# Kernel tuning notes

Hardware: AMD Instinct MI355X
Metric: run time of the kernel (lower is better)

The kernel has to match this reference:

```python
import jax, jax.numpy as jnp
import numpy as np

LN_EPS = 1e-5
NEG_INF = -1e30


def setup_inputs() -> dict:
    key = jax.random.key(0)
    k1, k2, k3 = jax.random.split(key, 3)
    B, N, D = 8192, 64, 64
    fi = jax.random.normal(k1, (B, N, D), dtype=jnp.float32)
    # orthogonal-init correlation matrix (matches nn.init.orthogonal_)
    a = jax.random.normal(k2, (D, D), dtype=jnp.float32)
    q, r = jnp.linalg.qr(a)
    correlation_mat = q * jnp.sign(jnp.diag(r))[None, :]
    ln1_gamma = jnp.ones((D,), dtype=jnp.float32)
    ln1_beta = jnp.zeros((D,), dtype=jnp.float32)
    last_w = jax.random.normal(k3, (1, 2 * D), dtype=jnp.float32) * 0.05
    last_b = jnp.zeros((1,), dtype=jnp.float32)
    return {"fi": fi, "correlation_mat": correlation_mat,
            "ln1_gamma": ln1_gamma, "ln1_beta": ln1_beta,
            "last_w": last_w, "last_b": last_b}


def _layer_norm(x, gamma, beta):
    mu = jnp.mean(x, axis=-1, keepdims=True)
    var = jnp.mean(jnp.square(x - mu), axis=-1, keepdims=True)
    return (x - mu) * jax.lax.rsqrt(var + LN_EPS) * gamma + beta


def reference(fi, correlation_mat, ln1_gamma, ln1_beta, last_w, last_b):
    B, N, D = fi.shape
    # pairwise bilinear scores: beta[b,i,j] = fi[b,i] @ C @ fi[b,j]
    fiC = jnp.einsum('bid,de->bie', fi, correlation_mat)        # [B,N,D]
    beta = jnp.einsum('bie,bje->bij', fiC, fi)                  # [B,N,N]
    # exclude self (i==j), matching the Python loop which skips j==i
    diag_mask = jnp.eye(N, dtype=bool)
    beta = jnp.where(diag_mask[None, :, :], NEG_INF, beta)
    alpha = jax.nn.softmax(beta, axis=-1)                       # [B,N,N]
    vi = jnp.einsum('bij,bjd->bid', alpha, fi)                  # [B,N,D]
    vi = jax.nn.relu(_layer_norm(vi, ln1_gamma, ln1_beta))
    all_inputs = jnp.concatenate([fi, vi], axis=-1)             # [B,N,2D]
    weight = jax.nn.sigmoid(jnp.einsum('bnk,ok->bno', all_inputs, last_w) + last_b)
    return weight  # [B, N, 1]
```

## Files before the change

### kernel.cpp

```cpp
#include <hip/hip_runtime.h>
#include <hip/hip_bf16.h>

typedef __attribute__((ext_vector_type(8))) short short8;
typedef __attribute__((ext_vector_type(4))) float floatx4;

constexpr float LN_EPS = 1e-5f;
constexpr float NEG_INF_V = -1e30f;

__device__ __forceinline__ unsigned int pk2(float a, float b) {
    float2 f2; f2.x = a; f2.y = b;
    __hip_bfloat162 h2 = __float22bfloat162_rn(f2);
    unsigned int u;
    __builtin_memcpy(&u, &h2, sizeof(u));
    return u;
}
__device__ __forceinline__ void splitpk(float a, float b,
                                        unsigned int& H, unsigned int& L) {
    H = pk2(a, b);
    const float ha = __builtin_bit_cast(float, H << 16);
    const float hb = __builtin_bit_cast(float, H & 0xFFFF0000u);
    L = pk2(a - ha, b - hb);
}

__device__ __forceinline__ int eoff(int r, int c) {
    return r * 64 + ((((c >> 3) ^ r) & 7) << 3) + (c & 7);
}
__device__ __forceinline__ int goff(int r, int g) {
    return r * 64 + (((g ^ r) & 7) << 3);
}

__device__ __forceinline__ float rsum16(float v) {
    v += __shfl_xor(v, 1, 64);
    v += __shfl_xor(v, 2, 64);
    v += __shfl_xor(v, 4, 64);
    v += __shfl_xor(v, 8, 64);
    return v;
}
__device__ __forceinline__ float rmax16(float v) {
    v = fmaxf(v, __shfl_xor(v, 1, 64));
    v = fmaxf(v, __shfl_xor(v, 2, 64));
    v = fmaxf(v, __shfl_xor(v, 4, 64));
    v = fmaxf(v, __shfl_xor(v, 8, 64));
    return v;
}

__global__ __launch_bounds__(256, 4)
void attn_mfma(const float* __restrict__ fi,
               const float* __restrict__ corr,
               const float* __restrict__ ln_g,
               const float* __restrict__ ln_b,
               const float* __restrict__ lw,
               const float* __restrict__ lb,
               float* __restrict__ out)
{
    __shared__ __align__(16) unsigned short sFiH[4096], sFiL[4096];
    __shared__ __align__(16) unsigned short sFtH[4096];
    __shared__ __align__(16) unsigned short sPH[4096], sPL[4096];

    const int tid  = threadIdx.x;
    const int lane = tid & 63;
    const int w    = tid >> 6;
    const int n    = lane & 15;
    const int quad = lane >> 4;
    const size_t blk = blockIdx.x;

    const int r = tid >> 2;
    const int a = tid & 3;
    float d0 = 0.f;
    {
        const float* fb = fi + blk * 4096 + (size_t)r * 64;
        #pragma unroll
        for (int i = 0; i < 4; ++i) {
            const int c = a * 4 + 16 * i;
            float4 v   = *(const float4*)(fb + c);
            float4 w0v = *(const float4*)&lw[c];
            d0 += v.x * w0v.x + v.y * w0v.y + v.z * w0v.z + v.w * w0v.w;
            unsigned int H01, L01, H23, L23;
            splitpk(v.x, v.y, H01, L01);
            splitpk(v.z, v.w, H23, L23);
            uint2 H = {H01, H23};
            uint2 L = {L01, L23};
            *(uint2*)&sFiH[eoff(r, c)] = H;
            *(uint2*)&sFiL[eoff(r, c)] = L;
            sFtH[eoff(c + 0, r)] = (unsigned short)H01;
            sFtH[eoff(c + 1, r)] = (unsigned short)(H01 >> 16);
            sFtH[eoff(c + 2, r)] = (unsigned short)H23;
            sFtH[eoff(c + 3, r)] = (unsigned short)(H23 >> 16);
        }
        d0 += __shfl_xor(d0, 1, 64);
        d0 += __shfl_xor(d0, 2, 64);
    }
    {
        const float* cb = corr + (size_t)r * 64;
        #pragma unroll
        for (int i = 0; i < 4; ++i) {
            const int c = a * 4 + 16 * i;
            float4 v = *(const float4*)(cb + c);
            unsigned int H01, L01, H23, L23;
            splitpk(v.x, v.y, H01, L01);
            splitpk(v.z, v.w, H23, L23);
            sPH[eoff(c + 0, r)] = (unsigned short)H01;
            sPH[eoff(c + 1, r)] = (unsigned short)(H01 >> 16);
            sPH[eoff(c + 2, r)] = (unsigned short)H23;
            sPH[eoff(c + 3, r)] = (unsigned short)(H23 >> 16);
            sPL[eoff(c + 0, r)] = (unsigned short)L01;
            sPL[eoff(c + 1, r)] = (unsigned short)(L01 >> 16);
            sPL[eoff(c + 2, r)] = (unsigned short)L23;
            sPL[eoff(c + 3, r)] = (unsigned short)(L23 >> 16);
        }
    }
    __syncthreads();

    const int arow = 16 * w + n;

    short8 Ah[2], Al[2];
    #pragma unroll
    for (int kk = 0; kk < 2; ++kk) {
        Ah[kk] = *(const short8*)&sFiH[goff(arow, kk * 4 + quad)];
        Al[kk] = *(const short8*)&sFiL[goff(arow, kk * 4 + quad)];
    }
    floatx4 acc1[4];
    #pragma unroll
    for (int t = 0; t < 4; ++t) {
        floatx4 acc = {0.f, 0.f, 0.f, 0.f};
        const int brow = 16 * t + n;
        #pragma unroll
        for (int kk = 0; kk < 2; ++kk) {
            short8 bh = *(const short8*)&sPH[goff(brow, kk * 4 + quad)];
            short8 bl = *(const short8*)&sPL[goff(brow, kk * 4 + quad)];
            acc = __builtin_amdgcn_mfma_f32_16x16x32_bf16(Ah[kk], bh, acc, 0, 0, 0);
            acc = __builtin_amdgcn_mfma_f32_16x16x32_bf16(Al[kk], bh, acc, 0, 0, 0);
            acc = __builtin_amdgcn_mfma_f32_16x16x32_bf16(Ah[kk], bl, acc, 0, 0, 0);
        }
        acc1[t] = acc;
    }

    __syncthreads();

    #pragma unroll
    for (int t = 0; t < 4; ++t) {
        const int col = 16 * t + n;
        const int row = 16 * w + quad * 4;
        unsigned int H01, L01, H23, L23;
        splitpk(acc1[t][0], acc1[t][1], H01, L01);
        splitpk(acc1[t][2], acc1[t][3], H23, L23);
        sPH[eoff(row + 0, col)] = (unsigned short)H01;
        sPH[eoff(row + 1, col)] = (unsigned short)(H01 >> 16);
        sPH[eoff(row + 2, col)] = (unsigned short)H23;
        sPH[eoff(row + 3, col)] = (unsigned short)(H23 >> 16);
        sPL[eoff(row + 0, col)] = (unsigned short)L01;
        sPL[eoff(row + 1, col)] = (unsigned short)(L01 >> 16);
        sPL[eoff(row + 2, col)] = (unsigned short)L23;
        sPL[eoff(row + 3, col)] = (unsigned short)(L23 >> 16);
    }

    short8 PAh[2], PAl[2];
    #pragma unroll
    for (int kk = 0; kk < 2; ++kk) {
        PAh[kk] = *(const short8*)&sPH[goff(arow, kk * 4 + quad)];
        PAl[kk] = *(const short8*)&sPL[goff(arow, kk * 4 + quad)];
    }
    floatx4 acc2[4];
    #pragma unroll
    for (int t = 0; t < 4; ++t) {
        floatx4 acc = {0.f, 0.f, 0.f, 0.f};
        const int brow = 16 * t + n;
        #pragma unroll
        for (int kk = 0; kk < 2; ++kk) {
            short8 bh = *(const short8*)&sFiH[goff(brow, kk * 4 + quad)];
            short8 bl = *(const short8*)&sFiL[goff(brow, kk * 4 + quad)];
            acc = __builtin_amdgcn_mfma_f32_16x16x32_bf16(PAh[kk], bh, acc, 0, 0, 0);
            acc = __builtin_amdgcn_mfma_f32_16x16x32_bf16(PAl[kk], bh, acc, 0, 0, 0);
            acc = __builtin_amdgcn_mfma_f32_16x16x32_bf16(PAh[kk], bl, acc, 0, 0, 0);
        }
        acc2[t] = acc;
    }

    #pragma unroll
    for (int reg = 0; reg < 4; ++reg) {
        const int row = 16 * w + quad * 4 + reg;
        float x[4];
        #pragma unroll
        for (int t = 0; t < 4; ++t) {
            x[t] = acc2[t][reg];
            if (row == 16 * t + n) x[t] = NEG_INF_V;
        }
        float m = fmaxf(fmaxf(x[0], x[1]), fmaxf(x[2], x[3]));
        m = rmax16(m);
        #pragma unroll
        for (int t = 0; t < 4; ++t) x[t] = __expf(x[t] - m);
        const unsigned int A01 = pk2(x[0], x[1]);
        const unsigned int A23 = pk2(x[2], x[3]);
        sPH[eoff(row, 0 + n)]  = (unsigned short)A01;
        sPH[eoff(row, 16 + n)] = (unsigned short)(A01 >> 16);
        sPH[eoff(row, 32 + n)] = (unsigned short)A23;
        sPH[eoff(row, 48 + n)] = (unsigned short)(A23 >> 16);
    }

    short8 AAh[2];
    #pragma unroll
    for (int kk = 0; kk < 2; ++kk)
        AAh[kk] = *(const short8*)&sPH[goff(arow, kk * 4 + quad)];
    floatx4 acc3[4];
    #pragma unroll
    for (int t = 0; t < 4; ++t) {
        floatx4 acc = {0.f, 0.f, 0.f, 0.f};
        const int brow = 16 * t + n;
        #pragma unroll
        for (int kk = 0; kk < 2; ++kk) {
            short8 bh = *(const short8*)&sFtH[goff(brow, kk * 4 + quad)];
            acc = __builtin_amdgcn_mfma_f32_16x16x32_bf16(AAh[kk], bh, acc, 0, 0, 0);
        }
        acc3[t] = acc;
    }

    float gv[4], bv[4], w1v[4];
    #pragma unroll
    for (int t = 0; t < 4; ++t) {
        gv[t]  = ln_g[16 * t + n];
        bv[t]  = ln_b[16 * t + n];
        w1v[t] = lw[64 + 16 * t + n];
    }
    const float bias = lb[0];
    float res[4];
    #pragma unroll
    for (int reg = 0; reg < 4; ++reg) {
        const int row16 = quad * 4 + reg;
        float s  = acc3[0][reg] + acc3[1][reg] + acc3[2][reg] + acc3[3][reg];
        float s2 = acc3[0][reg] * acc3[0][reg] + acc3[1][reg] * acc3[1][reg]
                 + acc3[2][reg] * acc3[2][reg] + acc3[3][reg] * acc3[3][reg];
        s  = rsum16(s);
        s2 = rsum16(s2);
        const float mu  = s * (1.0f / 64.0f);
        const float var = s2 * (1.0f / 64.0f) - mu * mu;
        const float rstd = __builtin_amdgcn_rsqf(var + LN_EPS);
        float dotp = 0.f;
        #pragma unroll
        for (int t = 0; t < 4; ++t) {
            float lnv = (acc3[t][reg] - mu) * rstd * gv[t] + bv[t];
            lnv = fmaxf(lnv, 0.f);
            dotp += lnv * w1v[t];
        }
        dotp = rsum16(dotp);
        const float d0row = __shfl(d0, row16 << 2, 64);
        res[reg] = __builtin_amdgcn_rcpf(1.0f + __expf(-(dotp + d0row + bias)));
    }
    if (n == 0) {
        float4 o = {res[0], res[1], res[2], res[3]};
        *(float4*)&out[blk * 64 + 16 * w + quad * 4] = o;
    }
}

extern "C" void kernel_launch(void* const* d_in, const int* in_sizes, int n_in,
                              void* d_out, int out_size, void* d_ws, size_t ws_size,
                              hipStream_t stream) {
    const float* fi   = (const float*)d_in[0];
    const float* corr = (const float*)d_in[1];
    const float* g    = (const float*)d_in[2];
    const float* b    = (const float*)d_in[3];
    const float* lw   = (const float*)d_in[4];
    const float* lb   = (const float*)d_in[5];
    float* out        = (float*)d_out;

    const int B = in_sizes[0] / 4096;
    hipLaunchKernelGGL(attn_mfma, dim3(B), dim3(256), 0, stream,
                       fi, corr, g, b, lw, lb, out);
}
```

Measured before the change: 224.6 us.

## Precompute split bf16 correlation fragments once and restructure fi staging

A tiny pre-kernel converts the correlation matrix into hi/lo bf16 MFMA fragment order in workspace, and each block reads those fragments straight from global/L2 instead of converting and staging corr in LDS. This removes one __syncthreads and the per-block corr conversion. The fi load is rewritten so each thread handles a 4x4 tile, using perm instructions to write the transposed copy as vector stores and computing row dot products locally. Shuffle-based 16-lane reductions become DPP row ops. The trade-off is an extra launch and per-lane global fragment loads in the first GEMM.

```diff
diff --git a/kernel.cpp b/kernel.cpp
--- a/kernel.cpp
+++ b/kernel.cpp
@@ -7,6 +7,15 @@
 constexpr float LN_EPS = 1e-5f;
 constexpr float NEG_INF_V = -1e30f;
 
+__device__ __forceinline__ unsigned short bf16hi_sw(float x) {
+    unsigned int u = __builtin_bit_cast(unsigned int, x);
+    u += 0x7FFFu + ((u >> 16) & 1u);
+    return (unsigned short)(u >> 16);
+}
+__device__ __forceinline__ float bf16f(unsigned short h) {
+    unsigned int u = ((unsigned int)h) << 16;
+    return __builtin_bit_cast(float, u);
+}
 __device__ __forceinline__ unsigned int pk2(float a, float b) {
     float2 f2; f2.x = a; f2.y = b;
     __hip_bfloat162 h2 = __float22bfloat162_rn(f2);
@@ -22,6 +31,36 @@
     L = pk2(a - ha, b - hb);
 }
 
+__device__ __forceinline__ unsigned int permlo(unsigned int A, unsigned int B) {
+    return __builtin_amdgcn_perm(B, A, 0x05040100u);
+}
+__device__ __forceinline__ unsigned int permhi(unsigned int A, unsigned int B) {
+    return __builtin_amdgcn_perm(B, A, 0x07060302u);
+}
+
+template<int CTRL>
+__device__ __forceinline__ float dppadd(float v) {
+    int t = __builtin_amdgcn_update_dpp(0, __builtin_bit_cast(int, v),
+                                        CTRL, 0xF, 0xF, true);
+    return v + __builtin_bit_cast(float, t);
+}
+template<int CTRL>
+__device__ __forceinline__ float dppmax(float v) {
+    int t = __builtin_amdgcn_update_dpp(0, __builtin_bit_cast(int, v),
+                                        CTRL, 0xF, 0xF, true);
+    return fmaxf(v, __builtin_bit_cast(float, t));
+}
+__device__ __forceinline__ float rsum16(float v) {
+    v = dppadd<0x121>(v); v = dppadd<0x122>(v);
+    v = dppadd<0x124>(v); v = dppadd<0x128>(v);
+    return v;
+}
+__device__ __forceinline__ float rmax16(float v) {
+    v = dppmax<0x121>(v); v = dppmax<0x122>(v);
+    v = dppmax<0x124>(v); v = dppmax<0x128>(v);
+    return v;
+}
+
 __device__ __forceinline__ int eoff(int r, int c) {
     return r * 64 + ((((c >> 3) ^ r) & 7) << 3) + (c & 7);
 }
@@ -29,24 +68,37 @@
     return r * 64 + (((g ^ r) & 7) << 3);
 }
 
-__device__ __forceinline__ float rsum16(float v) {
-    v += __shfl_xor(v, 1, 64);
-    v += __shfl_xor(v, 2, 64);
-    v += __shfl_xor(v, 4, 64);
-    v += __shfl_xor(v, 8, 64);
-    return v;
-}
-__device__ __forceinline__ float rmax16(float v) {
-    v = fmaxf(v, __shfl_xor(v, 1, 64));
-    v = fmaxf(v, __shfl_xor(v, 2, 64));
-    v = fmaxf(v, __shfl_xor(v, 4, 64));
-    v = fmaxf(v, __shfl_xor(v, 8, 64));
-    return v;
-}
-
+__global__ void prep_corr(const float* __restrict__ corr,
+                          unsigned short* __restrict__ ws) {
+    const int tid  = threadIdx.x;
+    const int lane = tid & 63;
+    const int t    = tid >> 6;
+    const int nn   = lane & 15;
+    const int q    = lane >> 4;
+    const int brow = 16 * t + nn;
+    #pragma unroll
+    for (int kk = 0; kk < 2; ++kk) {
+        const int kbase = (kk * 4 + q) * 8;
+        short8 H8, L8;
+        #pragma unroll
+        for (int e = 0; e < 8; ++e) {
+            const float v = corr[(kbase + e) * 64 + brow];
+            const unsigned short hh = bf16hi_sw(v);
+            const unsigned short ll = bf16hi_sw(v - bf16f(hh));
+            H8[e] = (short)hh;
+            L8[e] = (short)ll;
+        }
+        const int idx = ((t * 2 + kk) * 64 + lane) * 8;
+        *(short8*)&ws[idx]        = H8;
+        *(short8*)&ws[4096 + idx] = L8;
+    }
+}
+
+template<bool USEWS>
 __global__ __launch_bounds__(256, 4)
 void attn_mfma(const float* __restrict__ fi,
                const float* __restrict__ corr,
+               const unsigned short* __restrict__ wsC,
                const float* __restrict__ ln_g,
                const float* __restrict__ ln_b,
                const float* __restrict__ lw,
@@ -64,52 +116,75 @@
     const int quad = lane >> 4;
     const size_t blk = blockIdx.x;
 
-    const int r = tid >> 2;
-    const int a = tid & 3;
-    float d0 = 0.f;
+    const short8* wCH = (const short8*)wsC;
+    const short8* wCL = (const short8*)(wsC + 4096);
+
+    const int C = 4 * n;
+    const int R = 4 * (tid >> 4);
+    float d0v[4];
     {
-        const float* fb = fi + blk * 4096 + (size_t)r * 64;
+        const float* fb = fi + blk * 4096;
+        float4 v[4];
+        #pragma unroll
+        for (int i = 0; i < 4; ++i)
+            v[i] = *(const float4*)(fb + (R + i) * 64 + C);
+
+        const float4 w0v = *(const float4*)&lw[C];
         #pragma unroll
         for (int i = 0; i < 4; ++i) {
-            const int c = a * 4 + 16 * i;
-            float4 v   = *(const float4*)(fb + c);
-            float4 w0v = *(const float4*)&lw[c];
-            d0 += v.x * w0v.x + v.y * w0v.y + v.z * w0v.z + v.w * w0v.w;
-            unsigned int H01, L01, H23, L23;
-            splitpk(v.x, v.y, H01, L01);
-            splitpk(v.z, v.w, H23, L23);
-            uint2 H = {H01, H23};
-            uint2 L = {L01, L23};
-            *(uint2*)&sFiH[eoff(r, c)] = H;
-            *(uint2*)&sFiL[eoff(r, c)] = L;
-            sFtH[eoff(c + 0, r)] = (unsigned short)H01;
-            sFtH[eoff(c + 1, r)] = (unsigned short)(H01 >> 16);
-            sFtH[eoff(c + 2, r)] = (unsigned short)H23;
-            sFtH[eoff(c + 3, r)] = (unsigned short)(H23 >> 16);
-        }
-        d0 += __shfl_xor(d0, 1, 64);
-        d0 += __shfl_xor(d0, 2, 64);
-    }
-    {
-        const float* cb = corr + (size_t)r * 64;
+            float p = v[i].x * w0v.x + v[i].y * w0v.y
+                    + v[i].z * w0v.z + v[i].w * w0v.w;
+            d0v[i] = rsum16(p);
+        }
+
+        unsigned int H01[4], H23[4], L01[4], L23[4];
         #pragma unroll
         for (int i = 0; i < 4; ++i) {
-            const int c = a * 4 + 16 * i;
-            float4 v = *(const float4*)(cb + c);
-            unsigned int H01, L01, H23, L23;
-            splitpk(v.x, v.y, H01, L01);
-            splitpk(v.z, v.w, H23, L23);
-            sPH[eoff(c + 0, r)] = (unsigned short)H01;
-            sPH[eoff(c + 1, r)] = (unsigned short)(H01 >> 16);
-            sPH[eoff(c + 2, r)] = (unsigned short)H23;
-            sPH[eoff(c + 3, r)] = (unsigned short)(H23 >> 16);
-            sPL[eoff(c + 0, r)] = (unsigned short)L01;
-            sPL[eoff(c + 1, r)] = (unsigned short)(L01 >> 16);
-            sPL[eoff(c + 2, r)] = (unsigned short)L23;
-            sPL[eoff(c + 3, r)] = (unsigned short)(L23 >> 16);
-        }
-    }
-    __syncthreads();
+            splitpk(v[i].x, v[i].y, H01[i], L01[i]);
+            splitpk(v[i].z, v[i].w, H23[i], L23[i]);
+        }
+        #pragma unroll
+        for (int i = 0; i < 4; ++i) {
+            uint2 H = {H01[i], H23[i]};
+            uint2 L = {L01[i], L23[i]};
+            *(uint2*)&sFiH[eoff(R + i, C)] = H;
+            *(uint2*)&sFiL[eoff(R + i, C)] = L;
+        }
+        uint2 t0 = {permlo(H01[0], H01[1]), permlo(H01[2], H01[3])};
+        uint2 t1 = {permhi(H01[0], H01[1]), permhi(H01[2], H01[3])};
+        uint2 t2 = {permlo(H23[0], H23[1]), permlo(H23[2], H23[3])};
+        uint2 t3 = {permhi(H23[0], H23[1]), permhi(H23[2], H23[3])};
+        *(uint2*)&sFtH[eoff(C + 0, R)] = t0;
+        *(uint2*)&sFtH[eoff(C + 1, R)] = t1;
+        *(uint2*)&sFtH[eoff(C + 2, R)] = t2;
+        *(uint2*)&sFtH[eoff(C + 3, R)] = t3;
+    }
+
+    if constexpr (!USEWS) {
+        float4 cv[4];
+        #pragma unroll
+        for (int i = 0; i < 4; ++i)
+            cv[i] = *(const float4*)(corr + (size_t)(R + i) * 64 + C);
+        unsigned int cH01[4], cH23[4], cL01[4], cL23[4];
+        #pragma unroll
+        for (int i = 0; i < 4; ++i) {
+            splitpk(cv[i].x, cv[i].y, cH01[i], cL01[i]);
+            splitpk(cv[i].z, cv[i].w, cH23[i], cL23[i]);
+        }
+        uint2 h0 = {permlo(cH01[0], cH01[1]), permlo(cH01[2], cH01[3])};
+        uint2 h1 = {permhi(cH01[0], cH01[1]), permhi(cH01[2], cH01[3])};
+        uint2 h2 = {permlo(cH23[0], cH23[1]), permlo(cH23[2], cH23[3])};
+        uint2 h3 = {permhi(cH23[0], cH23[1]), permhi(cH23[2], cH23[3])};
+        uint2 l0 = {permlo(cL01[0], cL01[1]), permlo(cL01[2], cL01[3])};
+        uint2 l1 = {permhi(cL01[0], cL01[1]), permhi(cL01[2], cL01[3])};
+        uint2 l2 = {permlo(cL23[0], cL23[1]), permlo(cL23[2], cL23[3])};
+        uint2 l3 = {permhi(cL23[0], cL23[1]), permhi(cL23[2], cL23[3])};
+        *(uint2*)&sPH[eoff(C + 0, R)] = h0;  *(uint2*)&sPL[eoff(C + 0, R)] = l0;
+        *(uint2*)&sPH[eoff(C + 1, R)] = h1;  *(uint2*)&sPL[eoff(C + 1, R)] = l1;
+        *(uint2*)&sPH[eoff(C + 2, R)] = h2;  *(uint2*)&sPL[eoff(C + 2, R)] = l2;
+        *(uint2*)&sPH[eoff(C + 3, R)] = h3;  *(uint2*)&sPL[eoff(C + 3, R)] = l3;
+        __syncthreads();
+    }
 
     const int arow = 16 * w + n;
 
@@ -123,11 +198,18 @@
     #pragma unroll
     for (int t = 0; t < 4; ++t) {
         floatx4 acc = {0.f, 0.f, 0.f, 0.f};
-        const int brow = 16 * t + n;
         #pragma unroll
         for (int kk = 0; kk < 2; ++kk) {
-            short8 bh = *(const short8*)&sPH[goff(brow, kk * 4 + quad)];
-            short8 bl = *(const short8*)&sPL[goff(brow, kk * 4 + quad)];
+            short8 bh, bl;
+            if constexpr (USEWS) {
+                const int f = t * 2 + kk;
+                bh = wCH[f * 64 + lane];
+                bl = wCL[f * 64 + lane];
+            } else {
+                const int brow = 16 * t + n;
+                bh = *(const short8*)&sPH[goff(brow, kk * 4 + quad)];
+                bl = *(const short8*)&sPL[goff(brow, kk * 4 + quad)];
+            }
             acc = __builtin_amdgcn_mfma_f32_16x16x32_bf16(Ah[kk], bh, acc, 0, 0, 0);
             acc = __builtin_amdgcn_mfma_f32_16x16x32_bf16(Al[kk], bh, acc, 0, 0, 0);
             acc = __builtin_amdgcn_mfma_f32_16x16x32_bf16(Ah[kk], bl, acc, 0, 0, 0);
@@ -135,7 +217,7 @@
         acc1[t] = acc;
     }
 
-    __syncthreads();
+    if constexpr (!USEWS) __syncthreads();
 
     #pragma unroll
     for (int t = 0; t < 4; ++t) {
@@ -154,6 +236,8 @@
         sPL[eoff(row + 3, col)] = (unsigned short)(L23 >> 16);
     }
 
+    if constexpr (USEWS) __syncthreads();
+
     short8 PAh[2], PAl[2];
     #pragma unroll
     for (int kk = 0; kk < 2; ++kk) {
@@ -225,7 +309,6 @@
     float res[4];
     #pragma unroll
     for (int reg = 0; reg < 4; ++reg) {
-        const int row16 = quad * 4 + reg;
         float s  = acc3[0][reg] + acc3[1][reg] + acc3[2][reg] + acc3[3][reg];
         float s2 = acc3[0][reg] * acc3[0][reg] + acc3[1][reg] * acc3[1][reg]
                  + acc3[2][reg] * acc3[2][reg] + acc3[3][reg] * acc3[3][reg];
@@ -242,8 +325,7 @@
             dotp += lnv * w1v[t];
         }
         dotp = rsum16(dotp);
-        const float d0row = __shfl(d0, row16 << 2, 64);
-        res[reg] = __builtin_amdgcn_rcpf(1.0f + __expf(-(dotp + d0row + bias)));
+        res[reg] = __builtin_amdgcn_rcpf(1.0f + __expf(-(dotp + d0v[reg] + bias)));
     }
     if (n == 0) {
         float4 o = {res[0], res[1], res[2], res[3]};
@@ -263,6 +345,15 @@
     float* out        = (float*)d_out;
 
     const int B = in_sizes[0] / 4096;
-    hipLaunchKernelGGL(attn_mfma, dim3(B), dim3(256), 0, stream,
-                       fi, corr, g, b, lw, lb, out);
-}
+
+    if (d_ws != nullptr && ws_size >= 16384) {
+        unsigned short* wsC = (unsigned short*)d_ws;
+        hipLaunchKernelGGL(prep_corr, dim3(1), dim3(256), 0, stream, corr, wsC);
+        hipLaunchKernelGGL(HIP_KERNEL_NAME(attn_mfma<true>), dim3(B), dim3(256), 0,
+                           stream, fi, corr, wsC, g, b, lw, lb, out);
+    } else {
+        hipLaunchKernelGGL(HIP_KERNEL_NAME(attn_mfma<false>), dim3(B), dim3(256), 0,
+                           stream, fi, corr, (const unsigned short*)nullptr,
+                           g, b, lw, lb, out);
+    }
+}
```

Result: faster. 214.6 us (-4.5%).
